# Optimization experiments

Hardware: AMD Instinct MI355X
Metric: run time of the kernel (lower is better)

## Reference

```python
import jax, jax.numpy as jnp
import numpy as np

N_NODES = 50000


def _sage_conv(x, src, dst, Wl, Wr, b):
    # PyG SAGEConv (aggr='mean'): out = lin_l(mean_{j in N(i)} x_j) + lin_r(x_i)
    msgs = x[src]                                              # [E, d] gather
    s = jax.ops.segment_sum(msgs, dst, num_segments=N_NODES)   # [N, d]
    cnt = jax.ops.segment_sum(jnp.ones((src.shape[0], 1), x.dtype), dst,
                              num_segments=N_NODES)            # [N, 1]
    agg = s / jnp.maximum(cnt, 1.0)                            # mean, 0 if no nbrs
    return agg @ Wl.T + x @ Wr.T + b


def setup_inputs() -> dict:
    key = jax.random.key(0)
    ks = jax.random.split(key, 12)
    in_dim, h = 128, 128
    E, P = 500000, 200000
    x = jax.random.normal(ks[0], (N_NODES, in_dim), dtype=jnp.float32)
    edge_index = jax.random.randint(ks[1], (2, E), 0, N_NODES)
    pairs = jax.random.randint(ks[2], (P, 2), 0, N_NODES)
    def lin(k, fan_out, fan_in):
        bound = 1.0 / np.sqrt(fan_in)
        return jax.random.uniform(k, (fan_out, fan_in), jnp.float32, -bound, bound)
    return {
        "x": x, "edge_index": edge_index, "pairs": pairs,
        "Wl1": lin(ks[3], h, in_dim), "Wr1": lin(ks[4], h, in_dim),
        "b1": jnp.zeros((h,), jnp.float32),
        "Wl2": lin(ks[5], h, h), "Wr2": lin(ks[6], h, h),
        "b2": jnp.zeros((h,), jnp.float32),
        "W3": lin(ks[7], h, 2 * h), "b3": jnp.zeros((h,), jnp.float32),
        "W4": lin(ks[8], 1, h), "b4": jnp.zeros((1,), jnp.float32),
    }


def reference(x, edge_index, pairs, Wl1, Wr1, b1, Wl2, Wr2, b2, W3, b3, W4, b4):
    src, dst = edge_index[0], edge_index[1]
    h1 = jax.nn.relu(_sage_conv(x, src, dst, Wl1, Wr1, b1))    # [N, h]
    h2 = jax.nn.relu(_sage_conv(h1, src, dst, Wl2, Wr2, b2))   # [N, h]
    a = h2[pairs[:, 0]]                                        # [P, h]
    b = h2[pairs[:, 1]]                                        # [P, h]
    z = jnp.concatenate([a, b], axis=1)                        # [P, 2h]
    s = jax.nn.relu(z @ W3.T + b3) @ W4.T + b4                 # [P, 1]
    return jax.nn.sigmoid(s).squeeze(-1)                       # [P]
```

## Files before the change

kernel.cpp:

```cpp
#include <hip/hip_runtime.h>
#include <math.h>

#define N_NODES 50000
#define E_EDGES 500000
#define P_PAIRS 200000
#define MAX_DEG 64

#define NB        196
#define EB        2048
#define EPT       8
#define SORT_BLKS 245

typedef __bf16    bf16x8 __attribute__((ext_vector_type(8)));
typedef __bf16    bf16x4 __attribute__((ext_vector_type(4)));
typedef _Float16  f16x8  __attribute__((ext_vector_type(8)));
typedef float     f32x4  __attribute__((ext_vector_type(4)));


#define CONV_BLKS 1563
#define PREP_BLKS 128

__global__ __launch_bounds__(256) void pre_k(
        const float* __restrict__ x, __bf16* __restrict__ xb,
        const int* __restrict__ dst,
        int* __restrict__ bucketCnt, int* __restrict__ blockBase,
        const float* __restrict__ Wl1, const float* __restrict__ Wr1,
        const float* __restrict__ Wl2, const float* __restrict__ Wr2,
        const float* __restrict__ W3,
        __bf16* __restrict__ P1, __bf16* __restrict__ P2, __bf16* __restrict__ P4) {
    __shared__ int cnt[NB];
    int b = blockIdx.x, t = threadIdx.x;
    if (b < SORT_BLKS) {
        if (t < NB) cnt[t] = 0;
        __syncthreads();
        int ebase = b * EB;
        #pragma unroll
        for (int i = 0; i < EPT; ++i) {
            int e = ebase + i * 256 + t;
            if (e < E_EDGES) atomicAdd(&cnt[dst[e] >> 8], 1);
        }
        __syncthreads();
        if (t < NB) blockBase[b * NB + t] = atomicAdd(&bucketCnt[t], cnt[t]);
    } else if (b < SORT_BLKS + CONV_BLKS) {
        int i0 = (b - SORT_BLKS) * 1024 + t;
        #pragma unroll
        for (int k = 0; k < 4; ++k) {
            int i = i0 + k * 256;
            if (i < N_NODES * 128 / 4) {
                float4 v = ((const float4*)x)[i];
                bf16x4 o;
                o[0] = (__bf16)v.x; o[1] = (__bf16)v.y;
                o[2] = (__bf16)v.z; o[3] = (__bf16)v.w;
                *(bf16x4*)(xb + (size_t)i * 4) = o;
            }
        }
    } else {
        int i = (b - SORT_BLKS - CONV_BLKS) * 256 + t;
        int lane = (i >> 3) & 63;
        int j = i & 7;
        int kq = (lane >> 4) * 8 + j;
        {
            int kt = i >> 12, nt = (i >> 9) & 7;
            int n = nt * 16 + (lane & 15);
            int k = kt * 32 + kq;
            P1[i] = (__bf16)((k < 128) ? Wl1[n * 128 + k] : Wr1[n * 128 + (k - 128)]);
            P2[i] = (__bf16)((k < 128) ? Wl2[n * 128 + k] : Wr2[n * 128 + (k - 128)]);
        }
        {
            int kt = i >> 13, nt = (i >> 9) & 15;
            int n = nt * 16 + (lane & 15);
            int k = kt * 32 + kq;
            P4[i] = (__bf16)((n < 128) ? W3[n * 256 + k] : W3[(n - 128) * 256 + 128 + k]);
        }
    }
}


__global__ __launch_bounds__(256) void place_k(const int* __restrict__ src,
                                               const int* __restrict__ dst,
                                               const int* __restrict__ bucketCnt,
                                               const int* __restrict__ blockBase,
                                               unsigned* __restrict__ edgebuf) {
    __shared__ int cnt[256];
    __shared__ int buf[256];
    __shared__ int sbase[NB];
    __shared__ int gbase[NB];
    __shared__ int cur[NB];
    __shared__ unsigned sortbuf[EB];
    __shared__ unsigned char bktof[EB];
    int blk = blockIdx.x, t = threadIdx.x;

    int bv = (t < NB) ? bucketCnt[t] : 0;
    buf[t] = bv;
    __syncthreads();
    for (int off = 1; off < 256; off <<= 1) {
        int xv = (t >= off) ? buf[t - off] : 0;
        __syncthreads();
        buf[t] += xv;
        __syncthreads();
    }
    if (t < NB) gbase[t] = (buf[t] - bv) + blockBase[blk * NB + t];
    cnt[t] = 0;
    if (t < NB) cur[t] = 0;
    __syncthreads();

    unsigned packed[EPT];
    int bk[EPT];
    int ebase = blk * EB;
    #pragma unroll
    for (int i = 0; i < EPT; ++i) {
        int e = ebase + i * 256 + t;
        if (e < E_EDGES) {
            int d = dst[e];
            packed[i] = ((unsigned)d << 16) | (unsigned)src[e];
            bk[i] = d >> 8;
            atomicAdd(&cnt[bk[i]], 1);
        } else bk[i] = -1;
    }
    __syncthreads();

    int v = cnt[t];
    buf[t] = v;
    __syncthreads();
    for (int off = 1; off < 256; off <<= 1) {
        int xv = (t >= off) ? buf[t - off] : 0;
        __syncthreads();
        buf[t] += xv;
        __syncthreads();
    }
    if (t < NB) sbase[t] = buf[t] - v;
    __syncthreads();

    #pragma unroll
    for (int i = 0; i < EPT; ++i) {
        if (bk[i] >= 0) {
            int p = sbase[bk[i]] + atomicAdd(&cur[bk[i]], 1);
            sortbuf[p] = packed[i];
            bktof[p] = (unsigned char)bk[i];
        }
    }
    __syncthreads();

    int nE = E_EDGES - ebase; if (nE > EB) nE = EB;
    for (int i = t; i < nE; i += 256) {
        int bb = bktof[i];
        edgebuf[gbase[bb] + (i - sbase[bb])] = sortbuf[i];
    }
}


__global__ __launch_bounds__(256) void slots_k(const unsigned* __restrict__ edgebuf,
                                               const int* __restrict__ bucketCnt,
                                               unsigned short* __restrict__ slots,
                                               int* __restrict__ deg) {
    __shared__ unsigned short srow[256 * MAX_DEG];
    __shared__ int cur[256];
    __shared__ int buf[256];
    __shared__ int sc[2];
    int b = blockIdx.x, t = threadIdx.x;

    int bv = (t < NB) ? bucketCnt[t] : 0;
    buf[t] = bv;
    cur[t] = 0;
    __syncthreads();
    for (int off = 1; off < 256; off <<= 1) {
        int xv = (t >= off) ? buf[t - off] : 0;
        __syncthreads();
        buf[t] += xv;
        __syncthreads();
    }
    if (t == b) { sc[0] = buf[t] - bv; sc[1] = bv; }
    __syncthreads();
    int base = sc[0], n = sc[1];

    for (int i = t; i < n; i += 256) {
        unsigned p = edgebuf[base + i];
        int dl = (p >> 16) & 255;
        int pos = atomicAdd(&cur[dl], 1);
        if (pos < MAX_DEG) srow[dl * MAX_DEG + pos] = (unsigned short)(p & 0xFFFFu);
    }
    __syncthreads();
    const int4* sr16 = (const int4*)srow;
    int4* sl16 = (int4*)slots;
    int gbase16 = b * 2048;
    for (int i = t; i < 2048; i += 256) {
        int node = b * 256 + (i >> 3);
        if (node < N_NODES) sl16[gbase16 + i] = sr16[i];
    }
    int node = b * 256 + t;
    if (node < N_NODES) deg[node] = cur[t];
}


__global__ __launch_bounds__(256) void agg1_k(const __bf16* __restrict__ feat,
                                              const int* __restrict__ deg_a,
                                              const unsigned short* __restrict__ slots,
                                              __bf16* __restrict__ agg) {
    int n = blockIdx.x * 4 + (threadIdx.x >> 6);
    if (n >= N_NODES) return;
    int lane = threadIdx.x & 63;
    int slot = lane >> 4, l = lane & 15;
    int deg = deg_a[n];
    int nit = (deg < MAX_DEG) ? deg : MAX_DEG;

    int ed = (int)slots[n * MAX_DEG + lane];

    float s[8];
    #pragma unroll
    for (int e = 0; e < 8; ++e) s[e] = 0.f;

    int nv = (nit + 3) >> 2;
    int it = slot;
    while (nv > 0) {
        int take = (nv < 4) ? nv : 4;
        int sn0 = 0, sn1 = 0, sn2 = 0, sn3 = 0;
        bf16x8 v0{}, v1{}, v2{}, v3{};
        sn0 = __builtin_amdgcn_ds_bpermute(it << 2, ed);
        v0 = *(const bf16x8*)(feat + (size_t)sn0 * 128 + l * 8);
        if (take > 1) {
            sn1 = __builtin_amdgcn_ds_bpermute((it + 4) << 2, ed);
            v1 = *(const bf16x8*)(feat + (size_t)sn1 * 128 + l * 8);
        }
        if (take > 2) {
            sn2 = __builtin_amdgcn_ds_bpermute((it + 8) << 2, ed);
            v2 = *(const bf16x8*)(feat + (size_t)sn2 * 128 + l * 8);
        }
        if (take > 3) {
            sn3 = __builtin_amdgcn_ds_bpermute((it + 12) << 2, ed);
            v3 = *(const bf16x8*)(feat + (size_t)sn3 * 128 + l * 8);
        }
        if (it < nit) {
            #pragma unroll
            for (int e = 0; e < 8; ++e) s[e] += (float)v0[e];
        }
        if (take > 1 && it + 4 < nit) {
            #pragma unroll
            for (int e = 0; e < 8; ++e) s[e] += (float)v1[e];
        }
        if (take > 2 && it + 8 < nit) {
            #pragma unroll
            for (int e = 0; e < 8; ++e) s[e] += (float)v2[e];
        }
        if (take > 3 && it + 12 < nit) {
            #pragma unroll
            for (int e = 0; e < 8; ++e) s[e] += (float)v3[e];
        }
        it += 16;
        nv -= take;
    }

    #pragma unroll
    for (int e = 0; e < 8; ++e) {
        s[e] += __shfl_xor(s[e], 16, 64);
        s[e] += __shfl_xor(s[e], 32, 64);
    }

    if (slot == 0) {
        float inv = 1.0f / fmaxf((float)deg, 1.0f);
        bf16x8 o;
        #pragma unroll
        for (int e = 0; e < 8; ++e) o[e] = (__bf16)(s[e] * inv);
        *(bf16x8*)(agg + (size_t)n * 128 + l * 8) = o;
    }
}


__global__ __launch_bounds__(256) void layer_mfma_k(const __bf16* __restrict__ agg,
                                                    const __bf16* __restrict__ feat,
                                                    const __bf16* __restrict__ wpack,
                                                    const float* __restrict__ bias,
                                                    __bf16* __restrict__ out) {
    int wave = threadIdx.x >> 6;
    int lane = threadIdx.x & 63;
    int m = lane & 15, quad = lane >> 4;
    int rbase = blockIdx.x * 64 + wave * 16;
    int r0 = rbase + m; if (r0 > N_NODES - 1) r0 = N_NODES - 1;

    f32x4 acc[8];
    #pragma unroll
    for (int nt = 0; nt < 8; ++nt) acc[nt] = (f32x4)0.f;

    #pragma unroll
    for (int kt = 0; kt < 8; ++kt) {
        const __bf16* src = (kt < 4) ? agg : feat;
        int ko = (kt & 3) * 32 + quad * 8;
        bf16x8 a0 = *(const bf16x8*)(src + (size_t)r0 * 128 + ko);
        const __bf16* wb = wpack + (size_t)kt * 4096 + lane * 8;
        #pragma unroll
        for (int nt = 0; nt < 8; ++nt) {
            bf16x8 b = *(const bf16x8*)(wb + nt * 512);
            acc[nt] = __builtin_amdgcn_mfma_f32_16x16x32_bf16(a0, b, acc[nt], 0, 0, 0);
        }
    }

    #pragma unroll
    for (int r = 0; r < 4; ++r) {
        int row = rbase + quad * 4 + r;
        if (row < N_NODES) {
            #pragma unroll
            for (int nt = 0; nt < 8; ++nt) {
                float v = acc[nt][r] + bias[nt * 16 + m];
                out[(size_t)row * 128 + nt * 16 + m] = (__bf16)fmaxf(v, 0.f);
            }
        }
    }
}


__global__ __launch_bounds__(256) void layer2uv_k(const __bf16* __restrict__ agg,
                                                  const __bf16* __restrict__ feat,
                                                  const __bf16* __restrict__ wpack,
                                                  const float* __restrict__ bias,
                                                  const __bf16* __restrict__ wpack4,
                                                  _Float16* __restrict__ UV) {
    __shared__ __bf16 sh[4][16][136];
    int wave = threadIdx.x >> 6;
    int lane = threadIdx.x & 63;
    int m = lane & 15, q = lane >> 4;
    int rbase = blockIdx.x * 64 + wave * 16;
    int r0 = rbase + m; if (r0 > N_NODES - 1) r0 = N_NODES - 1;

    f32x4 acc[8];
    #pragma unroll
    for (int nt = 0; nt < 8; ++nt) acc[nt] = (f32x4)0.f;

    #pragma unroll
    for (int kt = 0; kt < 8; ++kt) {
        const __bf16* src = (kt < 4) ? agg : feat;
        int ko = (kt & 3) * 32 + q * 8;
        bf16x8 a0 = *(const bf16x8*)(src + (size_t)r0 * 128 + ko);
        const __bf16* wb = wpack + (size_t)kt * 4096 + lane * 8;
        #pragma unroll
        for (int nt = 0; nt < 8; ++nt) {
            bf16x8 b = *(const bf16x8*)(wb + nt * 512);
            acc[nt] = __builtin_amdgcn_mfma_f32_16x16x32_bf16(a0, b, acc[nt], 0, 0, 0);
        }
    }

    #pragma unroll
    for (int rr = 0; rr < 4; ++rr)
        #pragma unroll
        for (int nt = 0; nt < 8; ++nt) {
            float v = acc[nt][rr] + bias[nt * 16 + m];
            sh[wave][q * 4 + rr][nt * 16 + m] = (__bf16)fmaxf(v, 0.f);
        }

    f32x4 acc2[16];
    #pragma unroll
    for (int nt = 0; nt < 16; ++nt) acc2[nt] = (f32x4)0.f;

    #pragma unroll
    for (int kt = 0; kt < 4; ++kt) {
        bf16x8 a = *(const bf16x8*)&sh[wave][m][kt * 32 + q * 8];
        const __bf16* wb = wpack4 + (size_t)kt * 8192 + lane * 8;
        #pragma unroll
        for (int nt = 0; nt < 16; ++nt) {
            bf16x8 b = *(const bf16x8*)(wb + nt * 512);
            acc2[nt] = __builtin_amdgcn_mfma_f32_16x16x32_bf16(a, b, acc2[nt], 0, 0, 0);
        }
    }

    #pragma unroll
    for (int rr = 0; rr < 4; ++rr) {
        int row = rbase + q * 4 + rr;
        if (row < N_NODES) {
            #pragma unroll
            for (int nt = 0; nt < 16; ++nt)
                UV[(size_t)row * 256 + nt * 16 + m] = (_Float16)acc2[nt][rr];
        }
    }
}


__global__ __launch_bounds__(256) void pair_ep_k(const _Float16* __restrict__ UV,
                                                 const int* __restrict__ pairs,
                                                 const float* __restrict__ b3,
                                                 const float* __restrict__ W4,
                                                 const float* __restrict__ b4,
                                                 float* __restrict__ out) {
    int t = threadIdx.x;
    int g = t >> 4, l = t & 15;
    int base = blockIdx.x * 64;

    float4 b3a = *(const float4*)(b3 + l * 8);
    float4 b3b = *(const float4*)(b3 + l * 8 + 4);
    float4 w4a = *(const float4*)(W4 + l * 8);
    float4 w4b = *(const float4*)(W4 + l * 8 + 4);
    float bb[8] = {b3a.x, b3a.y, b3a.z, b3a.w, b3b.x, b3b.y, b3b.z, b3b.w};
    float ww[8] = {w4a.x, w4a.y, w4a.z, w4a.w, w4b.x, w4b.y, w4b.z, w4b.w};
    float b4s = b4[0];

    int2 pr[4];
    #pragma unroll
    for (int i = 0; i < 4; ++i) pr[i] = ((const int2*)pairs)[base + i * 16 + g];

    f16x8 ua[4], vb[4];
    #pragma unroll
    for (int i = 0; i < 4; ++i) {
        ua[i] = *(const f16x8*)(UV + (size_t)pr[i].x * 256 + l * 8);
        vb[i] = *(const f16x8*)(UV + (size_t)pr[i].y * 256 + 128 + l * 8);
    }

    #pragma unroll
    for (int i = 0; i < 4; ++i) {
        float p = 0.f;
        #pragma unroll
        for (int e = 0; e < 8; ++e)
            p += fmaxf((float)ua[i][e] + (float)vb[i][e] + bb[e], 0.f) * ww[e];
        #pragma unroll
        for (int s = 1; s < 16; s <<= 1) p += __shfl_xor(p, s, 64);
        if (l == 0)
            out[base + i * 16 + g] = 1.0f / (1.0f + expf(-(p + b4s)));
    }
}


extern "C" void kernel_launch(void* const* d_in, const int* in_sizes, int n_in,
                              void* d_out, int out_size, void* d_ws, size_t ws_size,
                              hipStream_t stream) {
    const float* x   = (const float*)d_in[0];
    const int*   ei  = (const int*)d_in[1];
    const int*   prs = (const int*)d_in[2];
    const float* Wl1 = (const float*)d_in[3];
    const float* Wr1 = (const float*)d_in[4];
    const float* b1  = (const float*)d_in[5];
    const float* Wl2 = (const float*)d_in[6];
    const float* Wr2 = (const float*)d_in[7];
    const float* b2  = (const float*)d_in[8];
    const float* W3  = (const float*)d_in[9];
    const float* b3  = (const float*)d_in[10];
    const float* W4  = (const float*)d_in[11];
    const float* b4  = (const float*)d_in[12];
    float* out = (float*)d_out;

    const int* srcv = ei;
    const int* dstv = ei + E_EDGES;

    char* ws = (char*)d_ws;
    size_t off = 0;
    auto alloc = [&](size_t bytes) -> void* {
        void* p = ws + off;
        off = (off + bytes + 255) & ~(size_t)255;
        return p;
    };
    int*            bucketCnt  = (int*)alloc(sizeof(int) * NB);
    int*            blockBase  = (int*)alloc(sizeof(int) * SORT_BLKS * NB);
    unsigned*       edgebuf    = (unsigned*)alloc(sizeof(unsigned) * E_EDGES);
    int*            deg        = (int*)alloc(sizeof(int) * N_NODES);
    unsigned short* slots      = (unsigned short*)alloc(sizeof(unsigned short) * (size_t)N_NODES * MAX_DEG + 512);
    __bf16*   P1     = (__bf16*)alloc(sizeof(__bf16) * 32768);
    __bf16*   P2     = (__bf16*)alloc(sizeof(__bf16) * 32768);
    __bf16*   P4     = (__bf16*)alloc(sizeof(__bf16) * 32768);
    __bf16*   xb     = (__bf16*)alloc(sizeof(__bf16) * (size_t)N_NODES * 128);
    __bf16*   aggb   = (__bf16*)alloc(sizeof(__bf16) * (size_t)N_NODES * 128);
    __bf16*   h1b    = (__bf16*)alloc(sizeof(__bf16) * (size_t)N_NODES * 128);
    _Float16* UV     = (_Float16*)alloc(sizeof(_Float16) * (size_t)N_NODES * 256);
    (void)ws_size; (void)in_sizes; (void)n_in; (void)out_size;

    hipMemsetAsync(bucketCnt, 0, sizeof(int) * NB, stream);

    pre_k<<<SORT_BLKS + CONV_BLKS + PREP_BLKS, 256, 0, stream>>>(
        x, xb, dstv, bucketCnt, blockBase, Wl1, Wr1, Wl2, Wr2, W3, P1, P2, P4);
    place_k<<<SORT_BLKS, 256, 0, stream>>>(srcv, dstv, bucketCnt, blockBase, edgebuf);
    slots_k<<<NB, 256, 0, stream>>>(edgebuf, bucketCnt, slots, deg);

    agg1_k<<<(N_NODES + 3) / 4, 256, 0, stream>>>(xb, deg, slots, aggb);
    layer_mfma_k<<<(N_NODES + 63) / 64, 256, 0, stream>>>(aggb, xb, P1, b1, h1b);
    agg1_k<<<(N_NODES + 3) / 4, 256, 0, stream>>>(h1b, deg, slots, aggb);
    layer2uv_k<<<(N_NODES + 63) / 64, 256, 0, stream>>>(aggb, h1b, P2, b2, P4, UV);
    pair_ep_k<<<P_PAIRS / 64, 256, 0, stream>>>(UV, prs, b3, W4, b4, out);
}
```

Measured before the change: 217.5 us.

## Fuse neighbor mean aggregation into SAGE layer MFMA kernels via shared memory

Merges the gather-mean aggregation kernel with the following MFMA linear layer for both SAGE layers. Each block of four waves now aggregates 16 nodes (four per wave) into shared memory, then the waves split the output columns of the 16-row GEMM tile. This drops the aggb intermediate write and read and two kernel launches. In exchange, each block does 4x less GEMM work per weight load, each wave aggregates its nodes one after another instead of one node per wave, and there are extra block-wide syncs.

```diff
diff --git a/kernel.cpp b/kernel.cpp
--- a/kernel.cpp
+++ b/kernel.cpp
@@ -192,181 +192,198 @@
 }
 
 
-__global__ __launch_bounds__(256) void agg1_k(const __bf16* __restrict__ feat,
-                                              const int* __restrict__ deg_a,
-                                              const unsigned short* __restrict__ slots,
-                                              __bf16* __restrict__ agg) {
-    int n = blockIdx.x * 4 + (threadIdx.x >> 6);
-    if (n >= N_NODES) return;
-    int lane = threadIdx.x & 63;
+__device__ __forceinline__ void agg_phase(const __bf16* __restrict__ feat,
+                                          const int* __restrict__ deg_a,
+                                          const unsigned short* __restrict__ slots,
+                                          int rbase, int wave, int lane,
+                                          __bf16 (* __restrict__ shA)[136]) {
     int slot = lane >> 4, l = lane & 15;
-    int deg = deg_a[n];
-    int nit = (deg < MAX_DEG) ? deg : MAX_DEG;
-
-    int ed = (int)slots[n * MAX_DEG + lane];
-
-    float s[8];
-    #pragma unroll
-    for (int e = 0; e < 8; ++e) s[e] = 0.f;
-
-    int nv = (nit + 3) >> 2;
-    int it = slot;
-    while (nv > 0) {
-        int take = (nv < 4) ? nv : 4;
-        int sn0 = 0, sn1 = 0, sn2 = 0, sn3 = 0;
-        bf16x8 v0{}, v1{}, v2{}, v3{};
-        sn0 = __builtin_amdgcn_ds_bpermute(it << 2, ed);
-        v0 = *(const bf16x8*)(feat + (size_t)sn0 * 128 + l * 8);
-        if (take > 1) {
-            sn1 = __builtin_amdgcn_ds_bpermute((it + 4) << 2, ed);
-            v1 = *(const bf16x8*)(feat + (size_t)sn1 * 128 + l * 8);
-        }
-        if (take > 2) {
-            sn2 = __builtin_amdgcn_ds_bpermute((it + 8) << 2, ed);
-            v2 = *(const bf16x8*)(feat + (size_t)sn2 * 128 + l * 8);
-        }
-        if (take > 3) {
-            sn3 = __builtin_amdgcn_ds_bpermute((it + 12) << 2, ed);
-            v3 = *(const bf16x8*)(feat + (size_t)sn3 * 128 + l * 8);
-        }
-        if (it < nit) {
+    int nb = rbase + wave * 4;
+    int dv = deg_a[nb + (lane & 3)];
+    int edv[4];
+    #pragma unroll
+    for (int i = 0; i < 4; ++i)
+        edv[i] = (int)slots[(size_t)(nb + i) * MAX_DEG + lane];
+
+    #pragma unroll
+    for (int i = 0; i < 4; ++i) {
+        int deg = __shfl(dv, i, 64);
+        int nit = (deg < MAX_DEG) ? deg : MAX_DEG;
+        float s[8];
+        #pragma unroll
+        for (int e = 0; e < 8; ++e) s[e] = 0.f;
+
+        int nv = (nit + 3) >> 2;
+        int it = slot;
+        while (nv > 0) {
+            int take = (nv < 4) ? nv : 4;
+            bf16x8 v0{}, v1{}, v2{}, v3{};
+            int sn0 = __builtin_amdgcn_ds_bpermute(it << 2, edv[i]);
+            v0 = *(const bf16x8*)(feat + (size_t)sn0 * 128 + l * 8);
+            if (take > 1) {
+                int sn1 = __builtin_amdgcn_ds_bpermute((it + 4) << 2, edv[i]);
+                v1 = *(const bf16x8*)(feat + (size_t)sn1 * 128 + l * 8);
+            }
+            if (take > 2) {
+                int sn2 = __builtin_amdgcn_ds_bpermute((it + 8) << 2, edv[i]);
+                v2 = *(const bf16x8*)(feat + (size_t)sn2 * 128 + l * 8);
+            }
+            if (take > 3) {
+                int sn3 = __builtin_amdgcn_ds_bpermute((it + 12) << 2, edv[i]);
+                v3 = *(const bf16x8*)(feat + (size_t)sn3 * 128 + l * 8);
+            }
+            if (it < nit) {
+                #pragma unroll
+                for (int e = 0; e < 8; ++e) s[e] += (float)v0[e];
+            }
+            if (take > 1 && it + 4 < nit) {
+                #pragma unroll
+                for (int e = 0; e < 8; ++e) s[e] += (float)v1[e];
+            }
+            if (take > 2 && it + 8 < nit) {
+                #pragma unroll
+                for (int e = 0; e < 8; ++e) s[e] += (float)v2[e];
+            }
+            if (take > 3 && it + 12 < nit) {
+                #pragma unroll
+                for (int e = 0; e < 8; ++e) s[e] += (float)v3[e];
+            }
+            it += 16;
+            nv -= take;
+        }
+
+        #pragma unroll
+        for (int e = 0; e < 8; ++e) {
+            s[e] += __shfl_xor(s[e], 16, 64);
+            s[e] += __shfl_xor(s[e], 32, 64);
+        }
+
+        if (slot == 0) {
+            float inv = 1.0f / fmaxf((float)deg, 1.0f);
+            bf16x8 o;
             #pragma unroll
-            for (int e = 0; e < 8; ++e) s[e] += (float)v0[e];
-        }
-        if (take > 1 && it + 4 < nit) {
-            #pragma unroll
-            for (int e = 0; e < 8; ++e) s[e] += (float)v1[e];
-        }
-        if (take > 2 && it + 8 < nit) {
-            #pragma unroll
-            for (int e = 0; e < 8; ++e) s[e] += (float)v2[e];
-        }
-        if (take > 3 && it + 12 < nit) {
-            #pragma unroll
-            for (int e = 0; e < 8; ++e) s[e] += (float)v3[e];
-        }
-        it += 16;
-        nv -= take;
-    }
-
-    #pragma unroll
-    for (int e = 0; e < 8; ++e) {
-        s[e] += __shfl_xor(s[e], 16, 64);
-        s[e] += __shfl_xor(s[e], 32, 64);
-    }
-
-    if (slot == 0) {
-        float inv = 1.0f / fmaxf((float)deg, 1.0f);
-        bf16x8 o;
-        #pragma unroll
-        for (int e = 0; e < 8; ++e) o[e] = (__bf16)(s[e] * inv);
-        *(bf16x8*)(agg + (size_t)n * 128 + l * 8) = o;
-    }
-}
-
-
-__global__ __launch_bounds__(256) void layer_mfma_k(const __bf16* __restrict__ agg,
-                                                    const __bf16* __restrict__ feat,
-                                                    const __bf16* __restrict__ wpack,
-                                                    const float* __restrict__ bias,
-                                                    __bf16* __restrict__ out) {
+            for (int e = 0; e < 8; ++e) o[e] = (__bf16)(s[e] * inv);
+            *(bf16x8*)&shA[wave * 4 + i][l * 8] = o;
+        }
+    }
+}
+
+
+__global__ __launch_bounds__(256) void fused_l1_k(const __bf16* __restrict__ feat,
+                                                  const int* __restrict__ deg_a,
+                                                  const unsigned short* __restrict__ slots,
+                                                  const __bf16* __restrict__ wpack,
+                                                  const float* __restrict__ bias,
+                                                  __bf16* __restrict__ out) {
+    __shared__ __bf16 shA[16][136];
     int wave = threadIdx.x >> 6;
     int lane = threadIdx.x & 63;
+    int rbase = blockIdx.x * 16;
+
+    agg_phase(feat, deg_a, slots, rbase, wave, lane, shA);
+    __syncthreads();
+
     int m = lane & 15, quad = lane >> 4;
-    int rbase = blockIdx.x * 64 + wave * 16;
-    int r0 = rbase + m; if (r0 > N_NODES - 1) r0 = N_NODES - 1;
-
-    f32x4 acc[8];
-    #pragma unroll
-    for (int nt = 0; nt < 8; ++nt) acc[nt] = (f32x4)0.f;
+    int r0 = rbase + m;
+    f32x4 acc[2];
+    acc[0] = (f32x4)0.f; acc[1] = (f32x4)0.f;
 
     #pragma unroll
     for (int kt = 0; kt < 8; ++kt) {
-        const __bf16* src = (kt < 4) ? agg : feat;
-        int ko = (kt & 3) * 32 + quad * 8;
-        bf16x8 a0 = *(const bf16x8*)(src + (size_t)r0 * 128 + ko);
+        bf16x8 a0;
+        if (kt < 4) a0 = *(const bf16x8*)&shA[m][kt * 32 + quad * 8];
+        else        a0 = *(const bf16x8*)(feat + (size_t)r0 * 128 + (kt & 3) * 32 + quad * 8);
         const __bf16* wb = wpack + (size_t)kt * 4096 + lane * 8;
         #pragma unroll
-        for (int nt = 0; nt < 8; ++nt) {
+        for (int j = 0; j < 2; ++j) {
+            int nt = wave * 2 + j;
             bf16x8 b = *(const bf16x8*)(wb + nt * 512);
-            acc[nt] = __builtin_amdgcn_mfma_f32_16x16x32_bf16(a0, b, acc[nt], 0, 0, 0);
-        }
-    }
-
-    #pragma unroll
-    for (int r = 0; r < 4; ++r) {
-        int row = rbase + quad * 4 + r;
-        if (row < N_NODES) {
-            #pragma unroll
-            for (int nt = 0; nt < 8; ++nt) {
-                float v = acc[nt][r] + bias[nt * 16 + m];
-                out[(size_t)row * 128 + nt * 16 + m] = (__bf16)fmaxf(v, 0.f);
-            }
-        }
-    }
-}
-
-
-__global__ __launch_bounds__(256) void layer2uv_k(const __bf16* __restrict__ agg,
-                                                  const __bf16* __restrict__ feat,
+            acc[j] = __builtin_amdgcn_mfma_f32_16x16x32_bf16(a0, b, acc[j], 0, 0, 0);
+        }
+    }
+
+    #pragma unroll
+    for (int j = 0; j < 2; ++j) {
+        int nt = wave * 2 + j;
+        #pragma unroll
+        for (int r = 0; r < 4; ++r) {
+            int row = rbase + quad * 4 + r;
+            float v = acc[j][r] + bias[nt * 16 + m];
+            out[(size_t)row * 128 + nt * 16 + m] = (__bf16)fmaxf(v, 0.f);
+        }
+    }
+}
+
+
+__global__ __launch_bounds__(256) void fused_l2_k(const __bf16* __restrict__ feat,
+                                                  const int* __restrict__ deg_a,
+                                                  const unsigned short* __restrict__ slots,
                                                   const __bf16* __restrict__ wpack,
                                                   const float* __restrict__ bias,
                                                   const __bf16* __restrict__ wpack4,
                                                   _Float16* __restrict__ UV) {
-    __shared__ __bf16 sh[4][16][136];
+    __shared__ __bf16 shA[16][136];
+    __shared__ __bf16 shH[16][136];
     int wave = threadIdx.x >> 6;
     int lane = threadIdx.x & 63;
+    int rbase = blockIdx.x * 16;
+
+    agg_phase(feat, deg_a, slots, rbase, wave, lane, shA);
+    __syncthreads();
+
     int m = lane & 15, q = lane >> 4;
-    int rbase = blockIdx.x * 64 + wave * 16;
-    int r0 = rbase + m; if (r0 > N_NODES - 1) r0 = N_NODES - 1;
-
-    f32x4 acc[8];
-    #pragma unroll
-    for (int nt = 0; nt < 8; ++nt) acc[nt] = (f32x4)0.f;
+    int r0 = rbase + m;
+    f32x4 acc[2];
+    acc[0] = (f32x4)0.f; acc[1] = (f32x4)0.f;
 
     #pragma unroll
     for (int kt = 0; kt < 8; ++kt) {
-        const __bf16* src = (kt < 4) ? agg : feat;
-        int ko = (kt & 3) * 32 + q * 8;
-        bf16x8 a0 = *(const bf16x8*)(src + (size_t)r0 * 128 + ko);
+        bf16x8 a0;
+        if (kt < 4) a0 = *(const bf16x8*)&shA[m][kt * 32 + q * 8];
+        else        a0 = *(const bf16x8*)(feat + (size_t)r0 * 128 + (kt & 3) * 32 + q * 8);
         const __bf16* wb = wpack + (size_t)kt * 4096 + lane * 8;
         #pragma unroll
-        for (int nt = 0; nt < 8; ++nt) {
+        for (int j = 0; j < 2; ++j) {
+            int nt = wave * 2 + j;
             bf16x8 b = *(const bf16x8*)(wb + nt * 512);
-            acc[nt] = __builtin_amdgcn_mfma_f32_16x16x32_bf16(a0, b, acc[nt], 0, 0, 0);
-        }
-    }
-
-    #pragma unroll
-    for (int rr = 0; rr < 4; ++rr)
-        #pragma unroll
-        for (int nt = 0; nt < 8; ++nt) {
-            float v = acc[nt][rr] + bias[nt * 16 + m];
-            sh[wave][q * 4 + rr][nt * 16 + m] = (__bf16)fmaxf(v, 0.f);
-        }
-
-    f32x4 acc2[16];
-    #pragma unroll
-    for (int nt = 0; nt < 16; ++nt) acc2[nt] = (f32x4)0.f;
+            acc[j] = __builtin_amdgcn_mfma_f32_16x16x32_bf16(a0, b, acc[j], 0, 0, 0);
+        }
+    }
+
+    #pragma unroll
+    for (int j = 0; j < 2; ++j) {
+        int nt = wave * 2 + j;
+        #pragma unroll
+        for (int rr = 0; rr < 4; ++rr) {
+            float v = acc[j][rr] + bias[nt * 16 + m];
+            shH[q * 4 + rr][nt * 16 + m] = (__bf16)fmaxf(v, 0.f);
+        }
+    }
+    __syncthreads();
+
+    f32x4 acc2[4];
+    #pragma unroll
+    for (int j = 0; j < 4; ++j) acc2[j] = (f32x4)0.f;
 
     #pragma unroll
     for (int kt = 0; kt < 4; ++kt) {
-        bf16x8 a = *(const bf16x8*)&sh[wave][m][kt * 32 + q * 8];
+        bf16x8 a = *(const bf16x8*)&shH[m][kt * 32 + q * 8];
         const __bf16* wb = wpack4 + (size_t)kt * 8192 + lane * 8;
         #pragma unroll
-        for (int nt = 0; nt < 16; ++nt) {
+        for (int j = 0; j < 4; ++j) {
+            int nt = wave * 4 + j;
             bf16x8 b = *(const bf16x8*)(wb + nt * 512);
-            acc2[nt] = __builtin_amdgcn_mfma_f32_16x16x32_bf16(a, b, acc2[nt], 0, 0, 0);
-        }
-    }
-
-    #pragma unroll
-    for (int rr = 0; rr < 4; ++rr) {
-        int row = rbase + q * 4 + rr;
-        if (row < N_NODES) {
-            #pragma unroll
-            for (int nt = 0; nt < 16; ++nt)
-                UV[(size_t)row * 256 + nt * 16 + m] = (_Float16)acc2[nt][rr];
+            acc2[j] = __builtin_amdgcn_mfma_f32_16x16x32_bf16(a, b, acc2[j], 0, 0, 0);
+        }
+    }
+
+    #pragma unroll
+    for (int j = 0; j < 4; ++j) {
+        int nt = wave * 4 + j;
+        #pragma unroll
+        for (int rr = 0; rr < 4; ++rr) {
+            int row = rbase + q * 4 + rr;
+            UV[(size_t)row * 256 + nt * 16 + m] = (_Float16)acc2[j][rr];
         }
     }
 }
@@ -452,7 +469,6 @@
     __bf16*   P2     = (__bf16*)alloc(sizeof(__bf16) * 32768);
     __bf16*   P4     = (__bf16*)alloc(sizeof(__bf16) * 32768);
     __bf16*   xb     = (__bf16*)alloc(sizeof(__bf16) * (size_t)N_NODES * 128);
-    __bf16*   aggb   = (__bf16*)alloc(sizeof(__bf16) * (size_t)N_NODES * 128);
     __bf16*   h1b    = (__bf16*)alloc(sizeof(__bf16) * (size_t)N_NODES * 128);
     _Float16* UV     = (_Float16*)alloc(sizeof(_Float16) * (size_t)N_NODES * 256);
     (void)ws_size; (void)in_sizes; (void)n_in; (void)out_size;
@@ -464,9 +480,7 @@
     place_k<<<SORT_BLKS, 256, 0, stream>>>(srcv, dstv, bucketCnt, blockBase, edgebuf);
     slots_k<<<NB, 256, 0, stream>>>(edgebuf, bucketCnt, slots, deg);
 
-    agg1_k<<<(N_NODES + 3) / 4, 256, 0, stream>>>(xb, deg, slots, aggb);
-    layer_mfma_k<<<(N_NODES + 63) / 64, 256, 0, stream>>>(aggb, xb, P1, b1, h1b);
-    agg1_k<<<(N_NODES + 3) / 4, 256, 0, stream>>>(h1b, deg, slots, aggb);
-    layer2uv_k<<<(N_NODES + 63) / 64, 256, 0, stream>>>(aggb, h1b, P2, b2, P4, UV);
+    fused_l1_k<<<N_NODES / 16, 256, 0, stream>>>(xb, deg, slots, P1, b1, h1b);
+    fused_l2_k<<<N_NODES / 16, 256, 0, stream>>>(h1b, deg, slots, P2, b2, P4, UV);
     pair_ep_k<<<P_PAIRS / 64, 256, 0, stream>>>(UV, prs, b3, W4, b4, out);
 }
```

After: 201.5 us, median of 2. 1.08x faster.
